# Optimization experiments

Hardware: AMD Instinct MI355X
Metric: run time of the kernel (lower is better)

Reference implementation:

```python
import jax, jax.numpy as jnp
import numpy as np

B, T, D, H = 4, 2048, 512, 8
DK = D // H


def setup_inputs() -> dict:
    key0 = jax.random.key(0)
    ks = jax.random.split(key0, 16)
    s = 1.0 / np.sqrt(D)
    inp = {
        "query": jax.random.normal(ks[0], (B, T, D), jnp.float32),
        "key": jax.random.normal(ks[1], (B, T, D), jnp.float32),
        "value": jax.random.normal(ks[2], (B, T, D), jnp.float32),
        "mask": jnp.ones((B, 1, T), jnp.int32),
        "pos_emb": jax.random.normal(ks[3], (1, T, D), jnp.float32),
        "Wq": jax.random.normal(ks[4], (D, D), jnp.float32) * s,
        "bq": jnp.zeros((D,), jnp.float32),
        "Wk": jax.random.normal(ks[5], (D, D), jnp.float32) * s,
        "bk": jnp.zeros((D,), jnp.float32),
        "Wv": jax.random.normal(ks[6], (D, D), jnp.float32) * s,
        "bv": jnp.zeros((D,), jnp.float32),
        "Wo": jax.random.normal(ks[7], (D, D), jnp.float32) * s,
        "bo": jnp.zeros((D,), jnp.float32),
        "Wp": jax.random.normal(ks[8], (D, D), jnp.float32) * s,  # linear_pos, no bias
        "pos_bias_u": jax.random.normal(ks[9], (H, DK), jnp.float32) * 0.05,
        "pos_bias_v": jax.random.normal(ks[10], (H, DK), jnp.float32) * 0.05,
    }
    return inp


def reference(query, key, value, mask, pos_emb, Wq, bq, Wk, bk, Wv, bv, Wo, bo, Wp, pos_bias_u, pos_bias_v):
    b, t1, d = query.shape
    h, dk = pos_bias_u.shape
    # projections -> (b, t, h, dk)
    q = (query @ Wq.T + bq).reshape(b, t1, h, dk)
    k = (key @ Wk.T + bk).reshape(b, -1, h, dk)
    v = (value @ Wv.T + bv).reshape(b, -1, h, dk)
    # positional projection (n_batch_pos == 1): (t2, h, dk)
    p = (pos_emb @ Wp.T).reshape(pos_emb.shape[0], -1, h, dk)[0]
    # content score (a+c) and position score (b+d); NOTE: this repo's forward
    # does not apply rel_shift -- matrix_bd is used directly.
    matrix_ac = jnp.einsum("bthd,bshd->bhts", q + pos_bias_u, k)
    matrix_bd = jnp.einsum("bthd,shd->bhts", q + pos_bias_v, p)
    scores = (matrix_ac + matrix_bd) / np.sqrt(dk)
    # mask: (b, 1, t2) -> (b, 1, 1, t2); masked where mask == 0
    m = (mask[:, None, :, :] == 0)
    scores = jnp.where(m, -jnp.inf, scores)
    attn = jax.nn.softmax(scores, axis=-1)
    attn = jnp.where(m, 0.0, attn)
    x = jnp.einsum("bhts,bshd->bthd", attn, v).reshape(b, t1, h * dk)
    return x @ Wo.T + bo
```

## Files before the change

kernel.cpp:

```cpp
#include <hip/hip_runtime.h>

typedef __bf16 bf16;
typedef __attribute__((ext_vector_type(8))) __bf16 bf16x8;
typedef __attribute__((ext_vector_type(4))) __bf16 bf16x4;
typedef __attribute__((ext_vector_type(4))) float f32x4;

#define NB 4
#define NT 2048
#define ND 512
#define NH 8
#define NDK 64
#define GAMMA 0.1803368801111204f

#define OFF_XQ 0ull
#define OFF_XK 4194304ull
#define OFF_XV 8388608ull
#define OFF_XP 12582912ull
#define OFF_WQ 13631488ull
#define OFF_WK 13893632ull
#define OFF_WV 14155776ull
#define OFF_WP 14417920ull
#define OFF_WO 14680064ull
#define OFF_QU 14942208ull
#define OFF_QV 19136512ull
#define OFF_KB 23330816ull
#define OFF_VT 27525120ull
#define OFF_PB 31719424ull
#define OFF_OA OFF_XQ

__global__ __launch_bounds__(256) void convert_bf16(
    const float* __restrict__ q, const float* __restrict__ k,
    const float* __restrict__ v, const float* __restrict__ p,
    const float* __restrict__ wq, const float* __restrict__ wk,
    const float* __restrict__ wv, const float* __restrict__ wp,
    const float* __restrict__ wo, bf16* __restrict__ dst) {
  int bid = blockIdx.x;
  const float* src;
  size_t doff;
  if (bid < 2048) { src = q; doff = OFF_XQ; }
  else if (bid < 4096) { src = k; doff = OFF_XK; bid -= 2048; }
  else if (bid < 6144) { src = v; doff = OFF_XV; bid -= 4096; }
  else if (bid < 6656) { src = p; doff = OFF_XP; bid -= 6144; }
  else if (bid < 6784) { src = wq; doff = OFF_WQ; bid -= 6656; }
  else if (bid < 6912) { src = wk; doff = OFF_WK; bid -= 6784; }
  else if (bid < 7040) { src = wv; doff = OFF_WV; bid -= 6912; }
  else if (bid < 7168) { src = wp; doff = OFF_WP; bid -= 7040; }
  else { src = wo; doff = OFF_WO; bid -= 7168; }
  size_t base = (size_t)bid * 2048 + threadIdx.x * 8;
  float4 x0 = *(const float4*)(src + base);
  float4 x1 = *(const float4*)(src + base + 4);
  bf16x8 o;
  o[0] = (bf16)x0.x; o[1] = (bf16)x0.y; o[2] = (bf16)x0.z; o[3] = (bf16)x0.w;
  o[4] = (bf16)x1.x; o[5] = (bf16)x1.y; o[6] = (bf16)x1.z; o[7] = (bf16)x1.w;
  *(bf16x8*)(dst + doff + base) = o;
}

__device__ __forceinline__ void flush_tile(const bf16* LT, bf16* dst, int bm,
                                           int bn, int tid, bool isP) {
#pragma unroll
  for (int i = 0; i < 8; i++) {
    int chunk = tid + i * 256;
    int mm = chunk >> 4, c8 = (chunk & 15) * 8;
    bf16x8 vv = *(const bf16x8*)&LT[mm * 144 + c8];
    int n = bn + c8, h = n >> 6, d = n & 63;
    int gm = bm + mm;
    size_t gidx;
    if (isP)
      gidx = ((size_t)h * NT + gm) * NDK + d;
    else
      gidx = ((size_t)((gm >> 11) * NH + h) * NT + (gm & 2047)) * NDK + d;
    *(bf16x8*)(dst + gidx) = vv;
  }
}

__global__ __launch_bounds__(256) void proj_fused(
    const bf16* __restrict__ Xq, const bf16* __restrict__ Xk,
    const bf16* __restrict__ Xv, const bf16* __restrict__ Xp,
    const bf16* __restrict__ wq, const bf16* __restrict__ wk,
    const bf16* __restrict__ wv, const bf16* __restrict__ wp,
    const float* __restrict__ bq, const float* __restrict__ bk,
    const float* __restrict__ bv, const float* __restrict__ pu,
    const float* __restrict__ pv, bf16* __restrict__ Qu, bf16* __restrict__ Qv,
    bf16* __restrict__ Kb, bf16* __restrict__ Vt, bf16* __restrict__ Pb) {
  __shared__ bf16 smem[2][128][72];

  const int bid = blockIdx.x;
  const int mode = (bid >= 768) ? 3 : (bid >> 8);
  const int idx = (mode == 3) ? bid - 768 : (bid & 255);
  const int bm = (idx >> 2) * 128, bn = (idx & 3) * 128;

  const bf16* X;
  const bf16* W;
  if (mode == 0) { X = Xq; W = wq; }
  else if (mode == 1) { X = Xk; W = wk; }
  else if (mode == 2) { X = Xv; W = wv; }
  else { X = Xp; W = wp; }

  const int tid = threadIdx.x;
  const int l = tid & 63, w = tid >> 6;
  const int q = l >> 4, ln = l & 15;
  const int wm = (w >> 1) * 64, wn = (w & 1) * 64;

  f32x4 acc[4][4];
#pragma unroll
  for (int i = 0; i < 4; i++)
#pragma unroll
    for (int j = 0; j < 4; j++) acc[i][j] = (f32x4){0.f, 0.f, 0.f, 0.f};

  const int srow = tid >> 3, scol = (tid & 7) * 8;
  const size_t abase = (size_t)(bm + srow) * 512 + scol;
  const size_t bbase = (size_t)(bn + srow) * 512 + scol;

  bf16x8 ar[4], br[4];
#pragma unroll
  for (int i = 0; i < 4; i++) {
    ar[i] = *(const bf16x8*)(X + abase + (size_t)i * 32 * 512);
    br[i] = *(const bf16x8*)(W + bbase + (size_t)i * 32 * 512);
  }

  for (int k0 = 0; k0 < 512; k0 += 64) {
    __syncthreads();
#pragma unroll
    for (int i = 0; i < 4; i++) {
      *(bf16x8*)&smem[0][srow + i * 32][scol] = ar[i];
      *(bf16x8*)&smem[1][srow + i * 32][scol] = br[i];
    }
    if (k0 + 64 < 512) {
#pragma unroll
      for (int i = 0; i < 4; i++) {
        ar[i] = *(const bf16x8*)(X + abase + k0 + 64 + (size_t)i * 32 * 512);
        br[i] = *(const bf16x8*)(W + bbase + k0 + 64 + (size_t)i * 32 * 512);
      }
    }
    __syncthreads();
#pragma unroll
    for (int kc = 0; kc < 2; kc++) {
      bf16x8 af[4], bfr[4];
#pragma unroll
      for (int rt = 0; rt < 4; rt++)
        af[rt] = *(const bf16x8*)&smem[0][wm + rt * 16 + ln][kc * 32 + q * 8];
#pragma unroll
      for (int ct = 0; ct < 4; ct++)
        bfr[ct] = *(const bf16x8*)&smem[1][wn + ct * 16 + ln][kc * 32 + q * 8];
#pragma unroll
      for (int rt = 0; rt < 4; rt++)
#pragma unroll
        for (int ct = 0; ct < 4; ct++)
          acc[rt][ct] = __builtin_amdgcn_mfma_f32_16x16x32_bf16(
              af[rt], bfr[ct], acc[rt][ct], 0, 0, 0);
    }
  }

  bf16* LT = &smem[0][0][0];

  if (mode == 2) {
    __syncthreads();
#pragma unroll
    for (int ct = 0; ct < 4; ct++) {
      const int n = bn + wn + ct * 16 + ln;
      const float bvn = bv[n];
#pragma unroll
      for (int rt = 0; rt < 4; rt++) {
        bf16x4 t4;
#pragma unroll
        for (int r = 0; r < 4; r++) t4[r] = (bf16)(acc[rt][ct][r] + bvn);
        *(bf16x4*)&LT[(wn + ct * 16 + ln) * 144 + wm + rt * 16 + q * 4] = t4;
      }
    }
    __syncthreads();
    const int b = bm >> 11, tb = bm & 2047;
#pragma unroll
    for (int i = 0; i < 8; i++) {
      int chunk = tid + i * 256;
      int nn = chunk >> 4, m8 = (chunk & 15) * 8;
      int n = bn + nn, h = n >> 6, d = n & 63;
      size_t gidx = (((size_t)(b * NH + h)) * NDK + d) * NT + tb + m8;
      *(bf16x8*)(Vt + gidx) = *(const bf16x8*)&LT[nn * 144 + m8];
    }
    return;
  }

  if (mode == 0) {
    float addu[4], addv[4];
#pragma unroll
    for (int ct = 0; ct < 4; ct++) {
      int n = bn + wn + ct * 16 + ln;
      float bb = bq[n];
      addu[ct] = bb + pu[n];
      addv[ct] = bb + pv[n];
    }
    __syncthreads();
#pragma unroll
    for (int rt = 0; rt < 4; rt++)
#pragma unroll
      for (int ct = 0; ct < 4; ct++)
#pragma unroll
        for (int r = 0; r < 4; r++)
          LT[(wm + rt * 16 + q * 4 + r) * 144 + wn + ct * 16 + ln] =
              (bf16)((acc[rt][ct][r] + addu[ct]) * GAMMA);
    __syncthreads();
    flush_tile(LT, Qu, bm, bn, tid, false);
    __syncthreads();
#pragma unroll
    for (int rt = 0; rt < 4; rt++)
#pragma unroll
      for (int ct = 0; ct < 4; ct++)
#pragma unroll
        for (int r = 0; r < 4; r++)
          LT[(wm + rt * 16 + q * 4 + r) * 144 + wn + ct * 16 + ln] =
              (bf16)((acc[rt][ct][r] + addv[ct]) * GAMMA);
    __syncthreads();
    flush_tile(LT, Qv, bm, bn, tid, false);
    return;
  }

  {
    float bb[4];
#pragma unroll
    for (int ct = 0; ct < 4; ct++) {
      int n = bn + wn + ct * 16 + ln;
      bb[ct] = (mode == 1) ? bk[n] : 0.f;
    }
    __syncthreads();
#pragma unroll
    for (int rt = 0; rt < 4; rt++)
#pragma unroll
      for (int ct = 0; ct < 4; ct++)
#pragma unroll
        for (int r = 0; r < 4; r++)
          LT[(wm + rt * 16 + q * 4 + r) * 144 + wn + ct * 16 + ln] =
              (bf16)(acc[rt][ct][r] + bb[ct]);
    __syncthreads();
    flush_tile(LT, (mode == 1) ? Kb : Pb, bm, bn, tid, mode == 3);
  }
}

__global__ __launch_bounds__(512) void flash(
    const bf16* __restrict__ Qu, const bf16* __restrict__ Qv,
    const bf16* __restrict__ Kb, const bf16* __restrict__ Pb,
    const bf16* __restrict__ Vt, const int* __restrict__ mask,
    bf16* __restrict__ Oa) {
  __shared__ bf16 sK[64][136];
  __shared__ bf16 sVt[64][72];
  __shared__ bf16 sPT[8][32][40];
  __shared__ float sbias[64];

  const int tid = threadIdx.x;
  const int l = tid & 63, wv = tid >> 6;
  const int q = l >> 4, ln = l & 15;
  const int t0 = blockIdx.x * 256;
  const int bh = blockIdx.y;
  const int b = bh >> 3;

  bf16x8 qf[2][4];
#pragma unroll
  for (int tt = 0; tt < 2; tt++) {
    const size_t qrow =
        (((size_t)bh) * NT + t0 + wv * 32 + tt * 16 + ln) * NDK;
    qf[tt][0] = *(const bf16x8*)(Qu + qrow + q * 8);
    qf[tt][1] = *(const bf16x8*)(Qu + qrow + 32 + q * 8);
    qf[tt][2] = *(const bf16x8*)(Qv + qrow + q * 8);
    qf[tt][3] = *(const bf16x8*)(Qv + qrow + 32 + q * 8);
  }

  int okacc = 1;
  for (int i = tid; i < NT; i += 512) okacc &= (mask[b * NT + i] != 0);
  const int allones = __syncthreads_and(okacc);

  float lsum[2] = {0.f, 0.f};
  f32x4 O[2][4];
#pragma unroll
  for (int tt = 0; tt < 2; tt++)
#pragma unroll
    for (int dt = 0; dt < 4; dt++) O[tt][dt] = (f32x4){0.f, 0.f, 0.f, 0.f};

  const bf16* Krow = Kb + ((size_t)bh) * NT * NDK;
  const bf16* Prow = Pb + ((size_t)(bh & 7)) * NT * NDK;
  const bf16* Vrow = Vt + ((size_t)bh) * NDK * NT;

  const int krow = tid >> 4, kcc = tid & 15;
  const int vrow = tid >> 3, vcol = (tid & 7) * 8;
  const bf16* kpsrc = (kcc < 8) ? (Krow + kcc * 8) : (Prow + (kcc - 8) * 8);

  bf16x8 rk[2], rv;
#pragma unroll
  for (int i = 0; i < 2; i++)
    rk[i] = *(const bf16x8*)(kpsrc + (size_t)(krow + i * 32) * NDK);
  rv = *(const bf16x8*)(Vrow + (size_t)vrow * NT + vcol);

  for (int s0 = 0; s0 < NT; s0 += 64) {
    __syncthreads();
#pragma unroll
    for (int i = 0; i < 2; i++) *(bf16x8*)&sK[krow + i * 32][kcc * 8] = rk[i];
    *(bf16x8*)&sVt[vrow][vcol] = rv;
    if (s0 + 64 < NT) {
#pragma unroll
      for (int i = 0; i < 2; i++)
        rk[i] =
            *(const bf16x8*)(kpsrc + (size_t)(s0 + 64 + krow + i * 32) * NDK);
      rv = *(const bf16x8*)(Vrow + (size_t)vrow * NT + s0 + 64 + vcol);
    }
    if (!allones && tid < 64)
      sbias[tid] = mask[b * NT + s0 + tid] ? 0.f : -1e30f;
    __syncthreads();

    f32x4 ST[2][4];
#pragma unroll
    for (int ct = 0; ct < 4; ct++) {
      ST[0][ct] = (f32x4){0.f, 0.f, 0.f, 0.f};
      ST[1][ct] = (f32x4){0.f, 0.f, 0.f, 0.f};
#pragma unroll
      for (int kc = 0; kc < 4; kc++) {
        bf16x8 kf = *(const bf16x8*)&sK[ct * 16 + ln][kc * 32 + q * 8];
        ST[0][ct] = __builtin_amdgcn_mfma_f32_16x16x32_bf16(kf, qf[0][kc],
                                                            ST[0][ct], 0, 0, 0);
        ST[1][ct] = __builtin_amdgcn_mfma_f32_16x16x32_bf16(kf, qf[1][kc],
                                                            ST[1][ct], 0, 0, 0);
      }
    }
    if (!allones) {
#pragma unroll
      for (int ct = 0; ct < 4; ct++) {
        float4 bb = *(const float4*)&sbias[ct * 16 + q * 4];
#pragma unroll
        for (int tt = 0; tt < 2; tt++) {
          ST[tt][ct][0] += bb.x;
          ST[tt][ct][1] += bb.y;
          ST[tt][ct][2] += bb.z;
          ST[tt][ct][3] += bb.w;
        }
      }
    }
#pragma unroll
    for (int c = 0; c < 2; c++) {
#pragma unroll
      for (int tt = 0; tt < 2; tt++) {
#pragma unroll
        for (int cc = 0; cc < 2; cc++) {
          const int ct = c * 2 + cc;
          unsigned u0 = __builtin_bit_cast(unsigned,
                                           __builtin_amdgcn_exp2f(ST[tt][ct][0]));
          unsigned u1 = __builtin_bit_cast(unsigned,
                                           __builtin_amdgcn_exp2f(ST[tt][ct][1]));
          unsigned u2 = __builtin_bit_cast(unsigned,
                                           __builtin_amdgcn_exp2f(ST[tt][ct][2]));
          unsigned u3 = __builtin_bit_cast(unsigned,
                                           __builtin_amdgcn_exp2f(ST[tt][ct][3]));
          lsum[tt] += __builtin_bit_cast(float, u0 & 0xffff0000u) +
                      __builtin_bit_cast(float, u1 & 0xffff0000u) +
                      __builtin_bit_cast(float, u2 & 0xffff0000u) +
                      __builtin_bit_cast(float, u3 & 0xffff0000u);
          uint2 pk;
          pk.x = (u0 >> 16) | (u1 & 0xffff0000u);
          pk.y = (u2 >> 16) | (u3 & 0xffff0000u);
          *(uint2*)&sPT[wv][tt * 16 + ln][cc * 16 + q * 4] = pk;
        }
      }
#pragma unroll
      for (int dt = 0; dt < 4; dt++) {
        bf16x8 vb = *(const bf16x8*)&sVt[dt * 16 + ln][c * 32 + q * 8];
#pragma unroll
        for (int tt = 0; tt < 2; tt++) {
          bf16x8 paf = *(const bf16x8*)&sPT[wv][tt * 16 + ln][q * 8];
          O[tt][dt] =
              __builtin_amdgcn_mfma_f32_16x16x32_bf16(paf, vb, O[tt][dt], 0, 0, 0);
        }
      }
    }
  }

#pragma unroll
  for (int tt = 0; tt < 2; tt++) {
    float s = lsum[tt];
    s += __shfl_xor(s, 16);
    s += __shfl_xor(s, 32);
#pragma unroll
    for (int r = 0; r < 4; r++) {
      float dr = __shfl(s, q * 4 + r);
      float inv = (dr > 0.f) ? 1.f / dr : 0.f;
      int t = t0 + wv * 32 + tt * 16 + q * 4 + r;
      size_t base = (((size_t)b * NT + t) * NH + (bh & 7)) * NDK;
#pragma unroll
      for (int dt = 0; dt < 4; dt++)
        Oa[base + dt * 16 + ln] = (bf16)(O[tt][dt][r] * inv);
    }
  }
}

__global__ __launch_bounds__(256) void out_gemm(const bf16* __restrict__ A,
                                                const bf16* __restrict__ W,
                                                const float* __restrict__ bias,
                                                float* __restrict__ out) {
  __shared__ bf16 sA[128][72];
  __shared__ bf16 sB[64][72];

  const int tid = threadIdx.x;
  const int l = tid & 63, w = tid >> 6;
  const int q = l >> 4, ln = l & 15;
  const int wm = (w >> 1) * 64, wn = (w & 1) * 32;
  const int bm = blockIdx.x * 128, bn = blockIdx.y * 64;

  f32x4 acc[4][2];
#pragma unroll
  for (int i = 0; i < 4; i++)
#pragma unroll
    for (int j = 0; j < 2; j++) acc[i][j] = (f32x4){0.f, 0.f, 0.f, 0.f};

  const int srow = tid >> 3, scol = (tid & 7) * 8;
  const size_t abase = (size_t)(bm + srow) * 512 + scol;
  const size_t bbase = (size_t)(bn + srow) * 512 + scol;

  bf16x8 ar[4], br[2];
#pragma unroll
  for (int i = 0; i < 4; i++)
    ar[i] = *(const bf16x8*)(A + abase + (size_t)i * 32 * 512);
#pragma unroll
  for (int i = 0; i < 2; i++)
    br[i] = *(const bf16x8*)(W + bbase + (size_t)i * 32 * 512);

  for (int k0 = 0; k0 < 512; k0 += 64) {
    __syncthreads();
#pragma unroll
    for (int i = 0; i < 4; i++) *(bf16x8*)&sA[srow + i * 32][scol] = ar[i];
#pragma unroll
    for (int i = 0; i < 2; i++) *(bf16x8*)&sB[srow + i * 32][scol] = br[i];
    if (k0 + 64 < 512) {
#pragma unroll
      for (int i = 0; i < 4; i++)
        ar[i] = *(const bf16x8*)(A + abase + k0 + 64 + (size_t)i * 32 * 512);
#pragma unroll
      for (int i = 0; i < 2; i++)
        br[i] = *(const bf16x8*)(W + bbase + k0 + 64 + (size_t)i * 32 * 512);
    }
    __syncthreads();
#pragma unroll
    for (int kc = 0; kc < 2; kc++) {
      bf16x8 af[4], bfr[2];
#pragma unroll
      for (int rt = 0; rt < 4; rt++)
        af[rt] = *(const bf16x8*)&sA[wm + rt * 16 + ln][kc * 32 + q * 8];
#pragma unroll
      for (int ct = 0; ct < 2; ct++)
        bfr[ct] = *(const bf16x8*)&sB[wn + ct * 16 + ln][kc * 32 + q * 8];
#pragma unroll
      for (int rt = 0; rt < 4; rt++)
#pragma unroll
        for (int ct = 0; ct < 2; ct++)
          acc[rt][ct] = __builtin_amdgcn_mfma_f32_16x16x32_bf16(
              af[rt], bfr[ct], acc[rt][ct], 0, 0, 0);
    }
  }

#pragma unroll
  for (int rt = 0; rt < 4; rt++)
#pragma unroll
    for (int ct = 0; ct < 2; ct++) {
      const int n = bn + wn + ct * 16 + ln;
      const float bias_n = bias[n];
#pragma unroll
      for (int r = 0; r < 4; r++) {
        const int m = bm + wm + rt * 16 + q * 4 + r;
        out[(size_t)m * 512 + n] = acc[rt][ct][r] + bias_n;
      }
    }
}

extern "C" void kernel_launch(void* const* d_in, const int* in_sizes, int n_in,
                              void* d_out, int out_size, void* d_ws,
                              size_t ws_size, hipStream_t stream) {
  const float* query = (const float*)d_in[0];
  const float* key = (const float*)d_in[1];
  const float* value = (const float*)d_in[2];
  const int* mask = (const int*)d_in[3];
  const float* pos = (const float*)d_in[4];
  const float* Wq = (const float*)d_in[5];
  const float* bq = (const float*)d_in[6];
  const float* Wk = (const float*)d_in[7];
  const float* bk = (const float*)d_in[8];
  const float* Wv = (const float*)d_in[9];
  const float* bv = (const float*)d_in[10];
  const float* Wo = (const float*)d_in[11];
  const float* bo = (const float*)d_in[12];
  const float* Wp = (const float*)d_in[13];
  const float* pu = (const float*)d_in[14];
  const float* pv = (const float*)d_in[15];
  float* out = (float*)d_out;

  bf16* ws = (bf16*)d_ws;
  dim3 blk(256);
  convert_bf16<<<dim3(7296), blk, 0, stream>>>(query, key, value, pos, Wq, Wk,
                                               Wv, Wp, Wo, ws);
  proj_fused<<<dim3(832), blk, 0, stream>>>(
      ws + OFF_XQ, ws + OFF_XK, ws + OFF_XV, ws + OFF_XP, ws + OFF_WQ,
      ws + OFF_WK, ws + OFF_WV, ws + OFF_WP, bq, bk, bv, pu, pv, ws + OFF_QU,
      ws + OFF_QV, ws + OFF_KB, ws + OFF_VT, ws + OFF_PB);
  flash<<<dim3(8, 32), dim3(512), 0, stream>>>(ws + OFF_QU, ws + OFF_QV,
                                               ws + OFF_KB, ws + OFF_PB,
                                               ws + OFF_VT, mask, ws + OFF_OA);
  out_gemm<<<dim3(64, 8), blk, 0, stream>>>(ws + OFF_OA, ws + OFF_WO, bo, out);
}
```

Measured before the change: 216.7 us.

## Feed softmax probabilities directly from registers into 16x16x16 MFMA for PV

In the flash kernel, the exponentiated scores are packed into registers and used directly as the A operand of 16x16x16 bf16 MFMAs. This removes the per-wave sPT shared-memory round trip that was needed to re-layout P for the 16x16x32 instruction. The cost is twice as many, smaller MFMA instructions for the PV product. Separately, the projection kernel swaps the MFMA operands for the non-V modes so each lane holds four contiguous output columns. Those lanes can then write bf16x4 vectors to the staging tile, whose row padding changes to 152, and load biases as float4.

```diff
diff --git a/kernel.cpp b/kernel.cpp
--- a/kernel.cpp
+++ b/kernel.cpp
@@ -4,6 +4,7 @@
 typedef __attribute__((ext_vector_type(8))) __bf16 bf16x8;
 typedef __attribute__((ext_vector_type(4))) __bf16 bf16x4;
 typedef __attribute__((ext_vector_type(4))) float f32x4;
+typedef __attribute__((ext_vector_type(4))) short s4;
 
 #define NB 4
 #define NT 2048
@@ -11,6 +12,7 @@
 #define NH 8
 #define NDK 64
 #define GAMMA 0.1803368801111204f
+#define LTS 152
 
 #define OFF_XQ 0ull
 #define OFF_XK 4194304ull
@@ -27,6 +29,18 @@
 #define OFF_VT 27525120ull
 #define OFF_PB 31719424ull
 #define OFF_OA OFF_XQ
+
+static __device__ __forceinline__ f32x4 mfma16b(s4 a, s4 b, f32x4 c) {
+#if __has_builtin(__builtin_amdgcn_mfma_f32_16x16x16bf16_1k)
+  return __builtin_amdgcn_mfma_f32_16x16x16bf16_1k(a, b, c, 0, 0, 0);
+#else
+  f32x4 d;
+  asm("v_mfma_f32_16x16x16_bf16 %0, %1, %2, %3"
+      : "=v"(d)
+      : "v"(a), "v"(b), "v"(c));
+  return d;
+#endif
+}
 
 __global__ __launch_bounds__(256) void convert_bf16(
     const float* __restrict__ q, const float* __restrict__ k,
@@ -61,7 +75,7 @@
   for (int i = 0; i < 8; i++) {
     int chunk = tid + i * 256;
     int mm = chunk >> 4, c8 = (chunk & 15) * 8;
-    bf16x8 vv = *(const bf16x8*)&LT[mm * 144 + c8];
+    bf16x8 vv = *(const bf16x8*)&LT[mm * LTS + c8];
     int n = bn + c8, h = n >> 6, d = n & 63;
     int gm = bm + mm;
     size_t gidx;
@@ -82,7 +96,7 @@
     const float* __restrict__ bv, const float* __restrict__ pu,
     const float* __restrict__ pv, bf16* __restrict__ Qu, bf16* __restrict__ Qv,
     bf16* __restrict__ Kb, bf16* __restrict__ Vt, bf16* __restrict__ Pb) {
-  __shared__ bf16 smem[2][128][72];
+  __shared__ bf16 smem[2][128][76];
 
   const int bid = blockIdx.x;
   const int mode = (bid >= 768) ? 3 : (bid >> 8);
@@ -142,12 +156,21 @@
 #pragma unroll
       for (int ct = 0; ct < 4; ct++)
         bfr[ct] = *(const bf16x8*)&smem[1][wn + ct * 16 + ln][kc * 32 + q * 8];
-#pragma unroll
-      for (int rt = 0; rt < 4; rt++)
-#pragma unroll
-        for (int ct = 0; ct < 4; ct++)
-          acc[rt][ct] = __builtin_amdgcn_mfma_f32_16x16x32_bf16(
-              af[rt], bfr[ct], acc[rt][ct], 0, 0, 0);
+      if (mode == 2) {
+#pragma unroll
+        for (int rt = 0; rt < 4; rt++)
+#pragma unroll
+          for (int ct = 0; ct < 4; ct++)
+            acc[rt][ct] = __builtin_amdgcn_mfma_f32_16x16x32_bf16(
+                af[rt], bfr[ct], acc[rt][ct], 0, 0, 0);
+      } else {
+#pragma unroll
+        for (int rt = 0; rt < 4; rt++)
+#pragma unroll
+          for (int ct = 0; ct < 4; ct++)
+            acc[rt][ct] = __builtin_amdgcn_mfma_f32_16x16x32_bf16(
+                bfr[ct], af[rt], acc[rt][ct], 0, 0, 0);
+      }
     }
   }
 
@@ -164,7 +187,7 @@
         bf16x4 t4;
 #pragma unroll
         for (int r = 0; r < 4; r++) t4[r] = (bf16)(acc[rt][ct][r] + bvn);
-        *(bf16x4*)&LT[(wn + ct * 16 + ln) * 144 + wm + rt * 16 + q * 4] = t4;
+        *(bf16x4*)&LT[(wn + ct * 16 + ln) * LTS + wm + rt * 16 + q * 4] = t4;
       }
     }
     __syncthreads();
@@ -175,61 +198,75 @@
       int nn = chunk >> 4, m8 = (chunk & 15) * 8;
       int n = bn + nn, h = n >> 6, d = n & 63;
       size_t gidx = (((size_t)(b * NH + h)) * NDK + d) * NT + tb + m8;
-      *(bf16x8*)(Vt + gidx) = *(const bf16x8*)&LT[nn * 144 + m8];
+      *(bf16x8*)(Vt + gidx) = *(const bf16x8*)&LT[nn * LTS + m8];
     }
     return;
   }
 
+  const int mloc = wm + ln;
+  const int nloc = wn + q * 4;
+
   if (mode == 0) {
-    float addu[4], addv[4];
+    float4 addu4[4], addv4[4];
 #pragma unroll
     for (int ct = 0; ct < 4; ct++) {
-      int n = bn + wn + ct * 16 + ln;
-      float bb = bq[n];
-      addu[ct] = bb + pu[n];
-      addv[ct] = bb + pv[n];
+      int n0 = bn + nloc + ct * 16;
+      float4 bb = *(const float4*)(bq + n0);
+      float4 uu = *(const float4*)(pu + n0);
+      float4 vv = *(const float4*)(pv + n0);
+      addu4[ct] = make_float4(bb.x + uu.x, bb.y + uu.y, bb.z + uu.z, bb.w + uu.w);
+      addv4[ct] = make_float4(bb.x + vv.x, bb.y + vv.y, bb.z + vv.z, bb.w + vv.w);
     }
     __syncthreads();
 #pragma unroll
     for (int rt = 0; rt < 4; rt++)
 #pragma unroll
-      for (int ct = 0; ct < 4; ct++)
+      for (int ct = 0; ct < 4; ct++) {
+        const float* au = &addu4[ct].x;
+        bf16x4 t4;
 #pragma unroll
         for (int r = 0; r < 4; r++)
-          LT[(wm + rt * 16 + q * 4 + r) * 144 + wn + ct * 16 + ln] =
-              (bf16)((acc[rt][ct][r] + addu[ct]) * GAMMA);
+          t4[r] = (bf16)((acc[rt][ct][r] + au[r]) * GAMMA);
+        *(bf16x4*)&LT[(mloc + rt * 16) * LTS + nloc + ct * 16] = t4;
+      }
     __syncthreads();
     flush_tile(LT, Qu, bm, bn, tid, false);
     __syncthreads();
 #pragma unroll
     for (int rt = 0; rt < 4; rt++)
 #pragma unroll
-      for (int ct = 0; ct < 4; ct++)
+      for (int ct = 0; ct < 4; ct++) {
+        const float* av = &addv4[ct].x;
+        bf16x4 t4;
 #pragma unroll
         for (int r = 0; r < 4; r++)
-          LT[(wm + rt * 16 + q * 4 + r) * 144 + wn + ct * 16 + ln] =
-              (bf16)((acc[rt][ct][r] + addv[ct]) * GAMMA);
+          t4[r] = (bf16)((acc[rt][ct][r] + av[r]) * GAMMA);
+        *(bf16x4*)&LT[(mloc + rt * 16) * LTS + nloc + ct * 16] = t4;
+      }
     __syncthreads();
     flush_tile(LT, Qv, bm, bn, tid, false);
     return;
   }
 
   {
-    float bb[4];
+    float4 bb4[4];
 #pragma unroll
     for (int ct = 0; ct < 4; ct++) {
-      int n = bn + wn + ct * 16 + ln;
-      bb[ct] = (mode == 1) ? bk[n] : 0.f;
+      int n0 = bn + nloc + ct * 16;
+      bb4[ct] = (mode == 1) ? *(const float4*)(bk + n0)
+                            : make_float4(0.f, 0.f, 0.f, 0.f);
     }
     __syncthreads();
 #pragma unroll
     for (int rt = 0; rt < 4; rt++)
 #pragma unroll
-      for (int ct = 0; ct < 4; ct++)
-#pragma unroll
-        for (int r = 0; r < 4; r++)
-          LT[(wm + rt * 16 + q * 4 + r) * 144 + wn + ct * 16 + ln] =
-              (bf16)(acc[rt][ct][r] + bb[ct]);
+      for (int ct = 0; ct < 4; ct++) {
+        const float* bbp = &bb4[ct].x;
+        bf16x4 t4;
+#pragma unroll
+        for (int r = 0; r < 4; r++) t4[r] = (bf16)(acc[rt][ct][r] + bbp[r]);
+        *(bf16x4*)&LT[(mloc + rt * 16) * LTS + nloc + ct * 16] = t4;
+      }
     __syncthreads();
     flush_tile(LT, (mode == 1) ? Kb : Pb, bm, bn, tid, mode == 3);
   }
@@ -242,7 +279,6 @@
     bf16* __restrict__ Oa) {
   __shared__ bf16 sK[64][136];
   __shared__ bf16 sVt[64][72];
-  __shared__ bf16 sPT[8][32][40];
   __shared__ float sbias[64];
 
   const int tid = threadIdx.x;
@@ -255,8 +291,7 @@
   bf16x8 qf[2][4];
 #pragma unroll
   for (int tt = 0; tt < 2; tt++) {
-    const size_t qrow =
-        (((size_t)bh) * NT + t0 + wv * 32 + tt * 16 + ln) * NDK;
+    const size_t qrow = (((size_t)bh) * NT + t0 + wv * 32 + tt * 16 + ln) * NDK;
     qf[tt][0] = *(const bf16x8*)(Qu + qrow + q * 8);
     qf[tt][1] = *(const bf16x8*)(Qu + qrow + 32 + q * 8);
     qf[tt][2] = *(const bf16x8*)(Qv + qrow + q * 8);
@@ -332,39 +367,32 @@
       }
     }
 #pragma unroll
-    for (int c = 0; c < 2; c++) {
+    for (int ct = 0; ct < 4; ct++) {
+      s4 pa[2];
 #pragma unroll
       for (int tt = 0; tt < 2; tt++) {
-#pragma unroll
-        for (int cc = 0; cc < 2; cc++) {
-          const int ct = c * 2 + cc;
-          unsigned u0 = __builtin_bit_cast(unsigned,
-                                           __builtin_amdgcn_exp2f(ST[tt][ct][0]));
-          unsigned u1 = __builtin_bit_cast(unsigned,
-                                           __builtin_amdgcn_exp2f(ST[tt][ct][1]));
-          unsigned u2 = __builtin_bit_cast(unsigned,
-                                           __builtin_amdgcn_exp2f(ST[tt][ct][2]));
-          unsigned u3 = __builtin_bit_cast(unsigned,
-                                           __builtin_amdgcn_exp2f(ST[tt][ct][3]));
-          lsum[tt] += __builtin_bit_cast(float, u0 & 0xffff0000u) +
-                      __builtin_bit_cast(float, u1 & 0xffff0000u) +
-                      __builtin_bit_cast(float, u2 & 0xffff0000u) +
-                      __builtin_bit_cast(float, u3 & 0xffff0000u);
-          uint2 pk;
-          pk.x = (u0 >> 16) | (u1 & 0xffff0000u);
-          pk.y = (u2 >> 16) | (u3 & 0xffff0000u);
-          *(uint2*)&sPT[wv][tt * 16 + ln][cc * 16 + q * 4] = pk;
-        }
+        unsigned u0 =
+            __builtin_bit_cast(unsigned, __builtin_amdgcn_exp2f(ST[tt][ct][0]));
+        unsigned u1 =
+            __builtin_bit_cast(unsigned, __builtin_amdgcn_exp2f(ST[tt][ct][1]));
+        unsigned u2 =
+            __builtin_bit_cast(unsigned, __builtin_amdgcn_exp2f(ST[tt][ct][2]));
+        unsigned u3 =
+            __builtin_bit_cast(unsigned, __builtin_amdgcn_exp2f(ST[tt][ct][3]));
+        lsum[tt] += __builtin_bit_cast(float, u0 & 0xffff0000u) +
+                    __builtin_bit_cast(float, u1 & 0xffff0000u) +
+                    __builtin_bit_cast(float, u2 & 0xffff0000u) +
+                    __builtin_bit_cast(float, u3 & 0xffff0000u);
+        uint2 pk;
+        pk.x = (u0 >> 16) | (u1 & 0xffff0000u);
+        pk.y = (u2 >> 16) | (u3 & 0xffff0000u);
+        pa[tt] = __builtin_bit_cast(s4, pk);
       }
 #pragma unroll
       for (int dt = 0; dt < 4; dt++) {
-        bf16x8 vb = *(const bf16x8*)&sVt[dt * 16 + ln][c * 32 + q * 8];
-#pragma unroll
-        for (int tt = 0; tt < 2; tt++) {
-          bf16x8 paf = *(const bf16x8*)&sPT[wv][tt * 16 + ln][q * 8];
-          O[tt][dt] =
-              __builtin_amdgcn_mfma_f32_16x16x32_bf16(paf, vb, O[tt][dt], 0, 0, 0);
-        }
+        s4 vb = *(const s4*)&sVt[dt * 16 + ln][ct * 16 + q * 4];
+        O[0][dt] = mfma16b(pa[0], vb, O[0][dt]);
+        O[1][dt] = mfma16b(pa[1], vb, O[1][dt]);
       }
     }
   }
```

Result: slower. 223.9 us (+3.3%).
